# Kernel tuning notes

Measured on AMD Instinct MI355X. Metric: run time of the kernel, lower is better.

Reference implementation:

```python
import jax, jax.numpy as jnp
import numpy as np

V, E, H, T = 50000, 256, 512, 64  # vocab, embed_dim, hidden_dim, n_tags
PAD = 0


def setup_inputs() -> dict:
    key = jax.random.key(0)
    ks = jax.random.split(key, 8)
    tokens = jax.random.randint(ks[0], (64, 512), 0, V, dtype=jnp.int64)
    emb = jax.random.normal(ks[1], (V, E), dtype=jnp.float32) * 0.05
    emb = emb.at[PAD].set(0.0)  # padding_idx row is zero
    W_ih = jax.random.normal(ks[2], (3 * H, E), dtype=jnp.float32) * 0.05
    W_hh = jax.random.normal(ks[3], (3 * H, H), dtype=jnp.float32) * 0.05
    b_ih = jax.random.normal(ks[4], (3 * H,), dtype=jnp.float32) * 0.05
    b_hh = jax.random.normal(ks[5], (3 * H,), dtype=jnp.float32) * 0.05
    W_tag = jax.random.normal(ks[6], (T, H), dtype=jnp.float32) * 0.05
    b_tag = jax.random.normal(ks[7], (T,), dtype=jnp.float32) * 0.05
    return {"tokens": tokens, "emb": emb, "W_ih": W_ih, "W_hh": W_hh,
            "b_ih": b_ih, "b_hh": b_hh, "W_tag": W_tag, "b_tag": b_tag}


def _gru_scan(x_tbE, W_ih, W_hh, b_ih, b_hh, h0):
    # x_tbE: [S, B, E] time-major embeddings. PyTorch GRUCell math.
    def step(h, x_t):
        gi = x_t @ W_ih.T + b_ih          # [B, 3H]
        gh = h @ W_hh.T + b_hh            # [B, 3H]
        r = jax.nn.sigmoid(gi[:, :H] + gh[:, :H])
        z = jax.nn.sigmoid(gi[:, H:2 * H] + gh[:, H:2 * H])
        n = jnp.tanh(gi[:, 2 * H:] + r * gh[:, 2 * H:])
        h_new = (1.0 - z) * n + z * h
        return h_new, h_new
    _, states = jax.lax.scan(step, h0, x_tbE)  # states: [S, B, H]
    return states


def reference(tokens, emb, W_ih, W_hh, b_ih, b_hh, W_tag, b_tag):
    B, S = tokens.shape
    embeds = emb[tokens]                          # [B, S, E]
    h0 = jnp.zeros((B, H), dtype=embeds.dtype)    # GRUCell default zero state
    states = _gru_scan(jnp.transpose(embeds, (1, 0, 2)), W_ih, W_hh, b_ih, b_hh, h0)
    states = jnp.transpose(states, (1, 0, 2))     # [B, S, H]
    tag_logits = states @ W_tag.T + b_tag         # [B, S, T]
    mask = (tokens != PAD)
    pred_tags = jnp.argmax(tag_logits, axis=-1)   # argmax(softmax) == argmax(logits)
    preds = pred_tags * mask
    return tag_logits, preds
```

## Files before the change

### kernel.cpp

```cpp
#include <hip/hip_runtime.h>


typedef unsigned short ushortT;
typedef unsigned long long u64c;
typedef float f32x4 __attribute__((ext_vector_type(4)));
typedef _Float16 f16x8 __attribute__((ext_vector_type(8)));
typedef unsigned int u32x4 __attribute__((ext_vector_type(4)));

#define MFMAH(a, b, c) __builtin_amdgcn_mfma_f32_16x16x32_f16((a), (b), (c), 0, 0, 0)
#define KSC (1.0f / 4096.0f)

__device__ __forceinline__ void splitf(float x, ushortT& hi, ushortT& lo) {
    _Float16 h = (_Float16)x;
    float r = x - (float)h;
    _Float16 l = (_Float16)(r * 4096.0f);
    hi = __builtin_bit_cast(ushortT, h);
    lo = __builtin_bit_cast(ushortT, l);
}

__global__ __launch_bounds__(256) void split_weights(
    const float* __restrict__ Whh, const float* __restrict__ Wih,
    const float* __restrict__ Wtag, ushortT* __restrict__ wh2,
    ushortT* __restrict__ wi2, ushortT* __restrict__ wt2)
{
    const int i = blockIdx.x * 256 + threadIdx.x;
    ushortT hi, lo;
    if (i < 786432) {
        splitf(Whh[i], hi, lo);
        wh2[i] = hi; wh2[786432 + i] = lo;
    } else if (i < 786432 + 393216) {
        const int j = i - 786432;
        splitf(Wih[j], hi, lo);
        wi2[j] = hi; wi2[393216 + j] = lo;
    } else if (i < 786432 + 393216 + 32768) {
        const int j = i - 786432 - 393216;
        splitf(Wtag[j], hi, lo);
        wt2[j] = hi; wt2[32768 + j] = lo;
    }
}

__global__ void init_ws(uint4* p, uint4* f) {
    int i = blockIdx.x * blockDim.x + threadIdx.x;
    uint4 z; z.x = 0u; z.y = 0u; z.z = 0u; z.w = 0u;
    if (i < 32768) p[i] = z;
    if (i < 256)   f[i] = z;
}

__global__ __launch_bounds__(512, 1) void gru_rec(
    const int* __restrict__ tok, const float* __restrict__ emb,
    const ushortT* __restrict__ wih2, const ushortT* __restrict__ whh2,
    const float* __restrict__ bih, const float* __restrict__ bhh,
    u64c* __restrict__ hbt, float* __restrict__ st,
    unsigned* __restrict__ flags)
{
    __shared__ ushortT xl[2][2][16][264];
    __shared__ unsigned hl[8256];
    __shared__ f32x4 pl[4][8][64];

    const int bid = blockIdx.x;
    const int cluster = bid >> 3;
    const int jg = bid & 7;
    const int tid = threadIdx.x;
    const int wave = tid >> 6;
    const int lane = tid & 63;
    const int wl = wave & 3;
    const bool upper = wave >= 4;
    const int ln = lane & 15, quad = lane >> 4;
    const int m0 = cluster * 16;
    const int j_lane = jg * 64 + wl * 16 + ln;

    unsigned* ownp = flags + (unsigned)(cluster * 8 + jg) * 32u;

    const float c_r  = bih[j_lane]        + bhh[j_lane];
    const float c_z  = bih[512 + j_lane]  + bhh[512 + j_lane];
    const float bi_n = bih[1024 + j_lane];
    const float bh_n = bhh[1024 + j_lane];

    const int xr = (tid & 255) >> 4, xc = (tid & 15) * 16;
    if (upper) {
        const int token = tok[(m0 + xr) * 512];
        const float* xsrc = emb + (size_t)token * 256 + xc;
#pragma unroll
        for (int i = 0; i < 16; ++i) {
            ushortT hi, lo; splitf(xsrc[i], hi, lo);
            xl[0][0][xr][xc + i] = hi; xl[0][1][xr][xc + i] = lo;
        }
    }
    __syncthreads();

    float hprev[4] = {0.f, 0.f, 0.f, 0.f};

    for (int t = 0; t < 512; ++t) {
        const int rb = t & 1;
        const int wb = rb ^ 1;
        u64c* tile = hbt + (size_t)rb * 32768 + (size_t)m0 * 512;

        f32x4 xv[4];
        if (upper) {
            const int tp = (t + 1) & 511;
            const int xtoken = tok[(m0 + xr) * 512 + tp];
            const float* xsrc = emb + (size_t)xtoken * 256 + xc;
#pragma unroll
            for (int i = 0; i < 4; ++i)
                xv[i] = *reinterpret_cast<const f32x4*>(xsrc + i * 4);
        }

        f32x4 m_r = (f32x4){0.f,0.f,0.f,0.f}, s_r = (f32x4){0.f,0.f,0.f,0.f};
        f32x4 m_z = (f32x4){0.f,0.f,0.f,0.f}, s_z = (f32x4){0.f,0.f,0.f,0.f};
        f32x4 m_gin = (f32x4){0.f,0.f,0.f,0.f}, s_gin = (f32x4){0.f,0.f,0.f,0.f};
        f32x4 m_ghn = (f32x4){0.f,0.f,0.f,0.f}, s_ghn = (f32x4){0.f,0.f,0.f,0.f};

        const int cks0 = upper ? 4 : 0;
#pragma unroll
        for (int ksi = 0; ksi < 4; ++ksi) {
            const int k = (cks0 + ksi) * 32 + quad * 8;
            f16x8 Axh = *reinterpret_cast<const f16x8*>(&xl[rb][0][ln][k]);
            f16x8 Axl = *reinterpret_cast<const f16x8*>(&xl[rb][1][ln][k]);
#pragma unroll
            for (int g = 0; g < 3; ++g) {
                const ushortT* wr = wih2 + (size_t)(g * 512 + j_lane) * 256 + k;
                f16x8 Wh = *reinterpret_cast<const f16x8*>(wr);
                f16x8 Wl = *reinterpret_cast<const f16x8*>(wr + 393216);
                if (g == 0) {
                    m_r = MFMAH(Axh, Wh, m_r);
                    s_r = MFMAH(Axl, Wh, s_r);
                    s_r = MFMAH(Axh, Wl, s_r);
                } else if (g == 1) {
                    m_z = MFMAH(Axh, Wh, m_z);
                    s_z = MFMAH(Axl, Wh, s_z);
                    s_z = MFMAH(Axh, Wl, s_z);
                } else {
                    m_gin = MFMAH(Axh, Wh, m_gin);
                    s_gin = MFMAH(Axl, Wh, s_gin);
                    s_gin = MFMAH(Axh, Wl, s_gin);
                }
            }
        }

        if (tid < 8) {
            const unsigned want = (unsigned)t;
            unsigned* pp = flags + (unsigned)(cluster * 8 + tid) * 32u;
            unsigned f = __hip_atomic_load(pp, __ATOMIC_RELAXED,
                                           __HIP_MEMORY_SCOPE_AGENT);
            while (f < want) {
                __builtin_amdgcn_s_sleep(2);
                f = __hip_atomic_load(pp, __ATOMIC_RELAXED,
                                      __HIP_MEMORY_SCOPE_AGENT);
            }
        }
        __syncthreads();

        u64c v[16];
#pragma unroll
        for (int j = 0; j < 16; ++j)
            v[j] = __hip_atomic_load(tile + tid + 512 * j,
                                     __ATOMIC_RELAXED, __HIP_MEMORY_SCOPE_AGENT);

        const unsigned etag = (unsigned)t;
        for (;;) {
            bool ok = true;
#pragma unroll
            for (int j = 0; j < 16; ++j) ok &= ((unsigned)(v[j] >> 32) == etag);
            if (__all(ok)) break;
            __builtin_amdgcn_s_sleep(4);
#pragma unroll
            for (int j = 0; j < 16; ++j)
                v[j] = __hip_atomic_load(tile + tid + 512 * j,
                                         __ATOMIC_RELAXED, __HIP_MEMORY_SCOPE_AGENT);
        }

#pragma unroll
        for (int j = 0; j < 16; ++j) {
            const int a = tid + 512 * j;
            hl[(a >> 9) * 516 + (a & 511)] = (unsigned)v[j];
        }
        __syncthreads();

        const int fks0 = upper ? 8 : 0;
#pragma unroll
        for (int ksi = 0; ksi < 8; ++ksi) {
            const int k = (fks0 + ksi) * 32 + quad * 8;
            const unsigned* hp = &hl[ln * 516 + k];
            u32x4 q0 = *reinterpret_cast<const u32x4*>(hp);
            u32x4 q1 = *reinterpret_cast<const u32x4*>(hp + 4);
            u32x4 ah, al;
#pragma unroll
            for (int i = 0; i < 2; ++i) {
                ah[i]   = (q0[2*i] & 0xffffu) | (q0[2*i+1] << 16);
                al[i]   = (q0[2*i] >> 16)     | (q0[2*i+1] & 0xffff0000u);
                ah[2+i] = (q1[2*i] & 0xffffu) | (q1[2*i+1] << 16);
                al[2+i] = (q1[2*i] >> 16)     | (q1[2*i+1] & 0xffff0000u);
            }
            f16x8 Ah = __builtin_bit_cast(f16x8, ah);
            f16x8 Al = __builtin_bit_cast(f16x8, al);
#pragma unroll
            for (int g = 0; g < 3; ++g) {
                const ushortT* wr = whh2 + (size_t)(g * 512 + j_lane) * 512 + k;
                f16x8 Wh = *reinterpret_cast<const f16x8*>(wr);
                f16x8 Wl = *reinterpret_cast<const f16x8*>(wr + 786432);
                if (g == 0) {
                    m_r = MFMAH(Ah, Wh, m_r);
                    s_r = MFMAH(Al, Wh, s_r);
                    s_r = MFMAH(Ah, Wl, s_r);
                } else if (g == 1) {
                    m_z = MFMAH(Ah, Wh, m_z);
                    s_z = MFMAH(Al, Wh, s_z);
                    s_z = MFMAH(Ah, Wl, s_z);
                } else {
                    m_ghn = MFMAH(Ah, Wh, m_ghn);
                    s_ghn = MFMAH(Al, Wh, s_ghn);
                    s_ghn = MFMAH(Ah, Wl, s_ghn);
                }
            }
        }

        if (upper) {
            const int u = wave - 4;
            pl[u][0][lane] = m_r;   pl[u][1][lane] = s_r;
            pl[u][2][lane] = m_z;   pl[u][3][lane] = s_z;
            pl[u][4][lane] = m_gin; pl[u][5][lane] = s_gin;
            pl[u][6][lane] = m_ghn; pl[u][7][lane] = s_ghn;
        }
        __syncthreads();

        float hn4[4];
        if (!upper) {
            m_r   += pl[wave][0][lane]; s_r   += pl[wave][1][lane];
            m_z   += pl[wave][2][lane]; s_z   += pl[wave][3][lane];
            m_gin += pl[wave][4][lane]; s_gin += pl[wave][5][lane];
            m_ghn += pl[wave][6][lane]; s_ghn += pl[wave][7][lane];

            u64c* hw = hbt + (size_t)wb * 32768;
            const u64c ntag = ((u64c)(unsigned)(t + 1)) << 32;
#pragma unroll
            for (int r4 = 0; r4 < 4; ++r4) {
                const float pre_r = m_r[r4] + s_r[r4] * KSC + c_r;
                const float pre_z = m_z[r4] + s_z[r4] * KSC + c_z;
                const float gin   = m_gin[r4] + s_gin[r4] * KSC + bi_n;
                const float ghn   = m_ghn[r4] + s_ghn[r4] * KSC + bh_n;
                const float rr = 1.f / (1.f + expf(-pre_r));
                const float zz = 1.f / (1.f + expf(-pre_z));
                const float nn = tanhf(gin + rr * ghn);
                const float hn = (1.f - zz) * nn + zz * hprev[r4];
                hprev[r4] = hn;
                hn4[r4] = hn;
                ushortT hi, lo; splitf(hn, hi, lo);
                const unsigned pk = (unsigned)hi | ((unsigned)lo << 16);
                const int b = m0 + quad * 4 + r4;
                __hip_atomic_store(&hw[b * 512 + j_lane], ntag | (u64c)pk,
                                   __ATOMIC_RELAXED, __HIP_MEMORY_SCOPE_AGENT);
            }
        } else {
#pragma unroll
            for (int i = 0; i < 16; ++i) {
                ushortT hi, lo; splitf(xv[i >> 2][i & 3], hi, lo);
                xl[wb][0][xr][xc + i] = hi; xl[wb][1][xr][xc + i] = lo;
            }
        }

        __syncthreads();
        if (tid == 0)
            __hip_atomic_store(ownp, (unsigned)(t + 1),
                               __ATOMIC_RELAXED, __HIP_MEMORY_SCOPE_AGENT);

        if (!upper) {
#pragma unroll
            for (int r4 = 0; r4 < 4; ++r4) {
                const int b = m0 + quad * 4 + r4;
                st[((size_t)b * 512 + t) * 512 + j_lane] = hn4[r4];
            }
        }
    }
}

__global__ __launch_bounds__(256) void tag_argmax(
    const float* __restrict__ st, const ushortT* __restrict__ wtag2,
    const float* __restrict__ btag, const int* __restrict__ tok,
    float* __restrict__ out)
{
    const int wave = threadIdx.x >> 6;
    const int lane = threadIdx.x & 63;
    const int ln = lane & 15, quad = lane >> 4;
    const int mt = blockIdx.x * 4 + wave;

    const float* arow = st + (size_t)(mt * 16 + ln) * 512;
    f32x4 am[4], as_[4];
#pragma unroll
    for (int ti = 0; ti < 4; ++ti) { am[ti] = (f32x4){0.f,0.f,0.f,0.f}; as_[ti] = (f32x4){0.f,0.f,0.f,0.f}; }

#pragma unroll
    for (int ks = 0; ks < 16; ++ks) {
        const int k = ks * 32 + quad * 8;
        f16x8 Ah, Al;
#pragma unroll
        for (int e = 0; e < 8; ++e) {
            const float x = arow[k + e];
            _Float16 h = (_Float16)x;
            Ah[e] = h;
            Al[e] = (_Float16)((x - (float)h) * 4096.0f);
        }
#pragma unroll
        for (int ti = 0; ti < 4; ++ti) {
            const ushortT* wr = wtag2 + (size_t)(ti * 16 + ln) * 512 + k;
            f16x8 Wh = *reinterpret_cast<const f16x8*>(wr);
            f16x8 Wl = *reinterpret_cast<const f16x8*>(wr + 32768);
            am[ti]  = MFMAH(Ah, Wh, am[ti]);
            as_[ti] = MFMAH(Ah, Wl, as_[ti]);
            as_[ti] = MFMAH(Al, Wh, as_[ti]);
        }
    }

    float vals[4][4];
#pragma unroll
    for (int ti = 0; ti < 4; ++ti) {
        const float bb = btag[ti * 16 + ln];
#pragma unroll
        for (int r = 0; r < 4; ++r) vals[ti][r] = am[ti][r] + as_[ti][r] * KSC + bb;
    }
#pragma unroll
    for (int ti = 0; ti < 4; ++ti)
#pragma unroll
        for (int r = 0; r < 4; ++r) {
            const int row = mt * 16 + quad * 4 + r;
            out[(size_t)row * 64 + ti * 16 + ln] = vals[ti][r];
        }
#pragma unroll
    for (int r = 0; r < 4; ++r) {
        float best = vals[0][r];
        int bc = ln;
#pragma unroll
        for (int ti = 1; ti < 4; ++ti) {
            const float v = vals[ti][r];
            const int c = ti * 16 + ln;
            if (v > best) { best = v; bc = c; }
        }
        for (int off = 1; off < 16; off <<= 1) {
            const float ov = __shfl_xor(best, off);
            const int oc = __shfl_xor(bc, off);
            if (ov > best || (ov == best && oc < bc)) { best = ov; bc = oc; }
        }
        if (ln == 0) {
            const int row = mt * 16 + quad * 4 + r;
            const int token = tok[row];
            const int pred = (token != 0) ? bc : 0;
            out[2097152 + (size_t)row] = (float)pred;
        }
    }
}

extern "C" void kernel_launch(void* const* d_in, const int* in_sizes, int n_in,
                              void* d_out, int out_size, void* d_ws, size_t ws_size,
                              hipStream_t stream) {
    const int*   tokens = (const int*)d_in[0];
    const float* emb    = (const float*)d_in[1];
    const float* Wih    = (const float*)d_in[2];
    const float* Whh    = (const float*)d_in[3];
    const float* bih    = (const float*)d_in[4];
    const float* bhh    = (const float*)d_in[5];
    const float* Wtag   = (const float*)d_in[6];
    const float* btag   = (const float*)d_in[7];

    char* ws = (char*)d_ws;
    u64c*     hbt   = (u64c*)ws;
    ushortT*  whh2  = (ushortT*)(ws + 524288);
    ushortT*  wih2  = (ushortT*)(ws + 3670016);
    ushortT*  wtag2 = (ushortT*)(ws + 5242880);
    float*    stf   = (float*)(ws + 5373952);
    float*    out   = (float*)d_out;

    unsigned* flags = (unsigned*)(out + 2097152);

    split_weights<<<4736, 256, 0, stream>>>(Whh, Wih, Wtag, whh2, wih2, wtag2);
    init_ws<<<128, 256, 0, stream>>>((uint4*)ws, (uint4*)flags);
    gru_rec<<<32, 512, 0, stream>>>(tokens, emb, wih2, whh2, bih, bhh, hbt, stf, flags);
    tag_argmax<<<512, 256, 0, stream>>>(stf, wtag2, btag, tokens, out);
}
```

Before: 7.312 ms.

## Keep W_hh high-half fragments in registers and split h into hi/lo LDS planes

Preloads the high-half fp16 W_hh fragments for each lane into 24 persistent f16x8 registers before the time loop, so only the low-half weights are still fetched from global memory every step. The shared h buffer is also stored as separate hi and lo fp16 planes, so the MFMA A operands load directly from LDS without per-element shift and mask repacking. The cost is 96 extra VGPRs per thread, which with 512-thread blocks risks spilling, and more scattered 16-bit LDS stores.

```diff
diff --git a/kernel.cpp b/kernel.cpp
--- a/kernel.cpp
+++ b/kernel.cpp
@@ -54,7 +54,8 @@
     unsigned* __restrict__ flags)
 {
     __shared__ ushortT xl[2][2][16][264];
-    __shared__ unsigned hl[8256];
+    __shared__ ushortT hlh[16 * 520];
+    __shared__ ushortT hll[16 * 520];
     __shared__ f32x4 pl[4][8][64];
 
     const int bid = blockIdx.x;
@@ -76,6 +77,20 @@
     const float bi_n = bih[1024 + j_lane];
     const float bh_n = bhh[1024 + j_lane];
 
+    const int fks0 = upper ? 8 : 0;
+    const int cks0 = upper ? 4 : 0;
+
+    f16x8 whhHi[24];
+#pragma unroll
+    for (int ksi = 0; ksi < 8; ++ksi) {
+        const int k = (fks0 + ksi) * 32 + quad * 8;
+#pragma unroll
+        for (int g = 0; g < 3; ++g)
+            whhHi[ksi * 3 + g] = *reinterpret_cast<const f16x8*>(
+                whh2 + (size_t)(g * 512 + j_lane) * 512 + k);
+    }
+    const ushortT* wlo = whh2 + 786432;
+
     const int xr = (tid & 255) >> 4, xc = (tid & 15) * 16;
     if (upper) {
         const int token = tok[(m0 + xr) * 512];
@@ -110,7 +125,6 @@
         f32x4 m_gin = (f32x4){0.f,0.f,0.f,0.f}, s_gin = (f32x4){0.f,0.f,0.f,0.f};
         f32x4 m_ghn = (f32x4){0.f,0.f,0.f,0.f}, s_ghn = (f32x4){0.f,0.f,0.f,0.f};
 
-        const int cks0 = upper ? 4 : 0;
 #pragma unroll
         for (int ksi = 0; ksi < 4; ++ksi) {
             const int k = (cks0 + ksi) * 32 + quad * 8;
@@ -171,33 +185,22 @@
 
 #pragma unroll
         for (int j = 0; j < 16; ++j) {
-            const int a = tid + 512 * j;
-            hl[(a >> 9) * 516 + (a & 511)] = (unsigned)v[j];
+            const unsigned pk = (unsigned)v[j];
+            hlh[j * 520 + tid] = (ushortT)(pk & 0xffffu);
+            hll[j * 520 + tid] = (ushortT)(pk >> 16);
         }
         __syncthreads();
 
-        const int fks0 = upper ? 8 : 0;
 #pragma unroll
         for (int ksi = 0; ksi < 8; ++ksi) {
             const int k = (fks0 + ksi) * 32 + quad * 8;
-            const unsigned* hp = &hl[ln * 516 + k];
-            u32x4 q0 = *reinterpret_cast<const u32x4*>(hp);
-            u32x4 q1 = *reinterpret_cast<const u32x4*>(hp + 4);
-            u32x4 ah, al;
-#pragma unroll
-            for (int i = 0; i < 2; ++i) {
-                ah[i]   = (q0[2*i] & 0xffffu) | (q0[2*i+1] << 16);
-                al[i]   = (q0[2*i] >> 16)     | (q0[2*i+1] & 0xffff0000u);
-                ah[2+i] = (q1[2*i] & 0xffffu) | (q1[2*i+1] << 16);
-                al[2+i] = (q1[2*i] >> 16)     | (q1[2*i+1] & 0xffff0000u);
-            }
-            f16x8 Ah = __builtin_bit_cast(f16x8, ah);
-            f16x8 Al = __builtin_bit_cast(f16x8, al);
+            f16x8 Ah = *reinterpret_cast<const f16x8*>(&hlh[ln * 520 + k]);
+            f16x8 Al = *reinterpret_cast<const f16x8*>(&hll[ln * 520 + k]);
 #pragma unroll
             for (int g = 0; g < 3; ++g) {
-                const ushortT* wr = whh2 + (size_t)(g * 512 + j_lane) * 512 + k;
-                f16x8 Wh = *reinterpret_cast<const f16x8*>(wr);
-                f16x8 Wl = *reinterpret_cast<const f16x8*>(wr + 786432);
+                f16x8 Wh = whhHi[ksi * 3 + g];
+                f16x8 Wl = *reinterpret_cast<const f16x8*>(
+                    wlo + (size_t)(g * 512 + j_lane) * 512 + k);
                 if (g == 0) {
                     m_r = MFMAH(Ah, Wh, m_r);
                     s_r = MFMAH(Al, Wh, s_r);
```

Result: no change. 7.237 ms (-1.0%).

## Drop per-element tags from hidden-state exchange and rely on block flags

Applied to the files above, without the earlier changes.

Hidden state is now exchanged between blocks as 32-bit packed hi/lo halves instead of 64-bit words carrying a step tag. The per-element tag polling loop is removed, so consumers trust only the per-block flag counters, which halves the global traffic for the exchange. Shared memory now holds hi and lo in separate planar arrays, which removes the unpacking shuffles before the MFMA operands. The producer's stores are relaxed atomics and the flag store is relaxed after a __syncthreads, with no release fence, so consumers may read stale hidden values. That is a memory-ordering correctness risk.

```diff
diff --git a/kernel.cpp b/kernel.cpp
--- a/kernel.cpp
+++ b/kernel.cpp
@@ -42,7 +42,7 @@
 __global__ void init_ws(uint4* p, uint4* f) {
     int i = blockIdx.x * blockDim.x + threadIdx.x;
     uint4 z; z.x = 0u; z.y = 0u; z.z = 0u; z.w = 0u;
-    if (i < 32768) p[i] = z;
+    if (i < 16384) p[i] = z;
     if (i < 256)   f[i] = z;
 }
 
@@ -50,11 +50,12 @@
     const int* __restrict__ tok, const float* __restrict__ emb,
     const ushortT* __restrict__ wih2, const ushortT* __restrict__ whh2,
     const float* __restrict__ bih, const float* __restrict__ bhh,
-    u64c* __restrict__ hbt, float* __restrict__ st,
+    unsigned* __restrict__ hb32, float* __restrict__ st,
     unsigned* __restrict__ flags)
 {
     __shared__ ushortT xl[2][2][16][264];
-    __shared__ unsigned hl[8256];
+    __shared__ ushortT hlh[16 * 520];
+    __shared__ ushortT hll[16 * 520];
     __shared__ f32x4 pl[4][8][64];
 
     const int bid = blockIdx.x;
@@ -76,6 +77,9 @@
     const float bi_n = bih[1024 + j_lane];
     const float bh_n = bhh[1024 + j_lane];
 
+    const int fks0 = upper ? 8 : 0;
+    const int cks0 = upper ? 4 : 0;
+
     const int xr = (tid & 255) >> 4, xc = (tid & 15) * 16;
     if (upper) {
         const int token = tok[(m0 + xr) * 512];
@@ -93,7 +97,8 @@
     for (int t = 0; t < 512; ++t) {
         const int rb = t & 1;
         const int wb = rb ^ 1;
-        u64c* tile = hbt + (size_t)rb * 32768 + (size_t)m0 * 512;
+        const u64c* tile64 =
+            (const u64c*)(hb32 + (size_t)rb * 32768 + (size_t)m0 * 512);
 
         f32x4 xv[4];
         if (upper) {
@@ -110,7 +115,6 @@
         f32x4 m_gin = (f32x4){0.f,0.f,0.f,0.f}, s_gin = (f32x4){0.f,0.f,0.f,0.f};
         f32x4 m_ghn = (f32x4){0.f,0.f,0.f,0.f}, s_ghn = (f32x4){0.f,0.f,0.f,0.f};
 
-        const int cks0 = upper ? 4 : 0;
 #pragma unroll
         for (int ksi = 0; ksi < 4; ++ksi) {
             const int k = (cks0 + ksi) * 32 + quad * 8;
@@ -150,49 +154,31 @@
         }
         __syncthreads();
 
-        u64c v[16];
-#pragma unroll
-        for (int j = 0; j < 16; ++j)
-            v[j] = __hip_atomic_load(tile + tid + 512 * j,
+        u64c v[8];
+#pragma unroll
+        for (int j = 0; j < 8; ++j)
+            v[j] = __hip_atomic_load(tile64 + tid + 512 * j,
                                      __ATOMIC_RELAXED, __HIP_MEMORY_SCOPE_AGENT);
 
-        const unsigned etag = (unsigned)t;
-        for (;;) {
-            bool ok = true;
-#pragma unroll
-            for (int j = 0; j < 16; ++j) ok &= ((unsigned)(v[j] >> 32) == etag);
-            if (__all(ok)) break;
-            __builtin_amdgcn_s_sleep(4);
-#pragma unroll
-            for (int j = 0; j < 16; ++j)
-                v[j] = __hip_atomic_load(tile + tid + 512 * j,
-                                         __ATOMIC_RELAXED, __HIP_MEMORY_SCOPE_AGENT);
-        }
-
-#pragma unroll
-        for (int j = 0; j < 16; ++j) {
+#pragma unroll
+        for (int j = 0; j < 8; ++j) {
             const int a = tid + 512 * j;
-            hl[(a >> 9) * 516 + (a & 511)] = (unsigned)v[j];
+            const int row = a >> 8;
+            const int c2 = (a & 255) * 2;
+            const unsigned lo32 = (unsigned)v[j];
+            const unsigned hi32 = (unsigned)(v[j] >> 32);
+            *reinterpret_cast<unsigned*>(&hlh[row * 520 + c2]) =
+                (lo32 & 0xffffu) | (hi32 << 16);
+            *reinterpret_cast<unsigned*>(&hll[row * 520 + c2]) =
+                (lo32 >> 16) | (hi32 & 0xffff0000u);
         }
         __syncthreads();
 
-        const int fks0 = upper ? 8 : 0;
 #pragma unroll
         for (int ksi = 0; ksi < 8; ++ksi) {
             const int k = (fks0 + ksi) * 32 + quad * 8;
-            const unsigned* hp = &hl[ln * 516 + k];
-            u32x4 q0 = *reinterpret_cast<const u32x4*>(hp);
-            u32x4 q1 = *reinterpret_cast<const u32x4*>(hp + 4);
-            u32x4 ah, al;
-#pragma unroll
-            for (int i = 0; i < 2; ++i) {
-                ah[i]   = (q0[2*i] & 0xffffu) | (q0[2*i+1] << 16);
-                al[i]   = (q0[2*i] >> 16)     | (q0[2*i+1] & 0xffff0000u);
-                ah[2+i] = (q1[2*i] & 0xffffu) | (q1[2*i+1] << 16);
-                al[2+i] = (q1[2*i] >> 16)     | (q1[2*i+1] & 0xffff0000u);
-            }
-            f16x8 Ah = __builtin_bit_cast(f16x8, ah);
-            f16x8 Al = __builtin_bit_cast(f16x8, al);
+            f16x8 Ah = *reinterpret_cast<const f16x8*>(&hlh[ln * 520 + k]);
+            f16x8 Al = *reinterpret_cast<const f16x8*>(&hll[ln * 520 + k]);
 #pragma unroll
             for (int g = 0; g < 3; ++g) {
                 const ushortT* wr = whh2 + (size_t)(g * 512 + j_lane) * 512 + k;
@@ -230,8 +216,7 @@
             m_gin += pl[wave][4][lane]; s_gin += pl[wave][5][lane];
             m_ghn += pl[wave][6][lane]; s_ghn += pl[wave][7][lane];
 
-            u64c* hw = hbt + (size_t)wb * 32768;
-            const u64c ntag = ((u64c)(unsigned)(t + 1)) << 32;
+            unsigned* hw32 = hb32 + (size_t)wb * 32768;
 #pragma unroll
             for (int r4 = 0; r4 < 4; ++r4) {
                 const float pre_r = m_r[r4] + s_r[r4] * KSC + c_r;
@@ -247,7 +232,7 @@
                 ushortT hi, lo; splitf(hn, hi, lo);
                 const unsigned pk = (unsigned)hi | ((unsigned)lo << 16);
                 const int b = m0 + quad * 4 + r4;
-                __hip_atomic_store(&hw[b * 512 + j_lane], ntag | (u64c)pk,
+                __hip_atomic_store(&hw32[b * 512 + j_lane], pk,
                                    __ATOMIC_RELAXED, __HIP_MEMORY_SCOPE_AGENT);
             }
         } else {
@@ -361,7 +346,7 @@
     const float* btag   = (const float*)d_in[7];
 
     char* ws = (char*)d_ws;
-    u64c*     hbt   = (u64c*)ws;
+    unsigned* hb32  = (unsigned*)ws;
     ushortT*  whh2  = (ushortT*)(ws + 524288);
     ushortT*  wih2  = (ushortT*)(ws + 3670016);
     ushortT*  wtag2 = (ushortT*)(ws + 5242880);
@@ -372,6 +357,6 @@
 
     split_weights<<<4736, 256, 0, stream>>>(Whh, Wih, Wtag, whh2, wih2, wtag2);
     init_ws<<<128, 256, 0, stream>>>((uint4*)ws, (uint4*)flags);
-    gru_rec<<<32, 512, 0, stream>>>(tokens, emb, wih2, whh2, bih, bhh, hbt, stf, flags);
+    gru_rec<<<32, 512, 0, stream>>>(tokens, emb, wih2, whh2, bih, bhh, hb32, stf, flags);
     tag_argmax<<<512, 256, 0, stream>>>(stf, wtag2, btag, tokens, out);
 }
```

After: 6.481 ms. 1.13x faster.
